# Kernel tuning notes

Measured on AMD Instinct MI355X. Metric: run time of the kernel, lower is better.

## Reference

```python
import jax, jax.numpy as jnp
import numpy as np

NUM_LOC = 20000
T = 24
IN_DIM = 18
H1 = 32
H2 = 32
GRU = 32
PW = 15
E_RAND = 640000


def setup_inputs() -> dict:
    key = jax.random.key(0)
    ks = jax.random.split(key, 32)
    # graph: random edges + self loops so every node has >=1 incoming edge
    edge_src = jnp.concatenate([
        jax.random.randint(ks[0], (E_RAND,), 0, NUM_LOC),
        jnp.arange(NUM_LOC)]).astype(jnp.int32)
    edge_dst = jnp.concatenate([
        jax.random.randint(ks[1], (E_RAND,), 0, NUM_LOC),
        jnp.arange(NUM_LOC)]).astype(jnp.int32)
    dynamic = jax.random.normal(ks[2], (NUM_LOC, T, IN_DIM), dtype=jnp.float32)
    cI = jax.random.uniform(ks[3], (T,), dtype=jnp.float32)
    cR = jax.random.uniform(ks[4], (T,), dtype=jnp.float32)
    I = jax.random.uniform(ks[5], (T,), dtype=jnp.float32)
    R = jax.random.uniform(ks[6], (T,), dtype=jnp.float32)
    N = jax.random.uniform(ks[7], (NUM_LOC, 1), dtype=jnp.float32) * 1e4 + 10.0
    h0 = jax.random.normal(ks[8], (1, GRU), dtype=jnp.float32) * 0.1
    s = 0.1
    # GAT layer 1 (torch Linear convention: weight [out, in], y = x @ W.T + b)
    W1 = jax.random.normal(ks[9], (H1, IN_DIM), dtype=jnp.float32) * s
    b1 = jnp.zeros((H1,), dtype=jnp.float32)
    aW1 = jax.random.normal(ks[10], (1, 2 * H1), dtype=jnp.float32) * s
    ab1 = jnp.zeros((1,), dtype=jnp.float32)
    # GAT layer 2
    W2 = jax.random.normal(ks[11], (H2, H1), dtype=jnp.float32) * s
    b2 = jnp.zeros((H2,), dtype=jnp.float32)
    aW2 = jax.random.normal(ks[12], (1, 2 * H2), dtype=jnp.float32) * s
    ab2 = jnp.zeros((1,), dtype=jnp.float32)
    # GRUCell
    Wih = jax.random.normal(ks[13], (3 * GRU, H2), dtype=jnp.float32) * s
    Whh = jax.random.normal(ks[14], (3 * GRU, GRU), dtype=jnp.float32) * s
    bih = jnp.zeros((3 * GRU,), dtype=jnp.float32)
    bhh = jnp.zeros((3 * GRU,), dtype=jnp.float32)
    # output heads
    WI = jax.random.normal(ks[15], (PW, GRU + 2), dtype=jnp.float32) * s
    bI = jnp.zeros((PW,), dtype=jnp.float32)
    WR = jax.random.normal(ks[16], (PW, GRU + 2), dtype=jnp.float32) * s
    bR = jnp.zeros((PW,), dtype=jnp.float32)
    Ws = jax.random.normal(ks[17], (2, GRU + 2), dtype=jnp.float32) * s
    bs = jnp.zeros((2,), dtype=jnp.float32)
    return {"dynamic": dynamic, "cI": cI, "cR": cR, "N": N, "I": I, "R": R,
            "h0": h0, "W1": W1, "b1": b1, "aW1": aW1, "ab1": ab1,
            "W2": W2, "b2": b2, "aW2": aW2, "ab2": ab2,
            "Wih": Wih, "Whh": Whh, "bih": bih, "bhh": bhh,
            "WI": WI, "bI": bI, "WR": WR, "bR": bR, "Ws": Ws, "bs": bs,
            "edge_src": edge_src, "edge_dst": edge_dst}


def _gat(x, W, b, aW, ab, src, dst):
    # z = fc(x); per-edge attention e = leaky_relu(attn_fc([z_src, z_dst]))
    z = x @ W.T + b                                        # [n, out]
    e = jax.nn.leaky_relu(
        (jnp.concatenate([z[src], z[dst]], axis=1) @ aW.T + ab)[:, 0])  # [E]
    # softmax over incoming edges per destination node
    m = jax.ops.segment_max(e, dst, num_segments=NUM_LOC)
    ex = jnp.exp(e - m[dst])
    den = jax.ops.segment_sum(ex, dst, num_segments=NUM_LOC)
    alpha = ex / den[dst]
    return jax.ops.segment_sum(alpha[:, None] * z[src], dst, num_segments=NUM_LOC)


def reference(dynamic, cI, cR, N, I, R, h0,
              W1, b1, aW1, ab1, W2, b2, aW2, ab2,
              Wih, Whh, bih, bhh, WI, bI, WR, bR, Ws, bs,
              edge_src, edge_dst):
    Nv = N[:, 0]                                          # [num_loc]

    def step(h, inp):
        x_t, cI_t, cR_t, I_t, R_t = inp
        c = jax.nn.elu(_gat(x_t, W1, b1, aW1, ab1, edge_src, edge_dst))
        c = jax.nn.elu(_gat(c, W2, b2, aW2, ab2, edge_src, edge_dst))
        pooled = jnp.max(c, axis=0)[None, :]              # [1, H2]
        # GRUCell
        gi = pooled @ Wih.T + bih
        gh = h @ Whh.T + bhh
        r = jax.nn.sigmoid(gi[:, :GRU] + gh[:, :GRU])
        zg = jax.nn.sigmoid(gi[:, GRU:2 * GRU] + gh[:, GRU:2 * GRU])
        n = jnp.tanh(gi[:, 2 * GRU:] + r * gh[:, 2 * GRU:])
        h_new = (1.0 - zg) * n + zg * h                   # [1, GRU]
        hc = jnp.concatenate([h_new, cI_t.reshape(1, 1), cR_t.reshape(1, 1)], axis=1)
        pred_I = hc @ WI.T + bI                           # [1, PW]
        pred_R = hc @ WR.T + bR
        sir = hc @ Ws.T + bs                              # [1, 2]
        alpha = jax.nn.sigmoid(sir[0, 0])
        beta = jax.nn.sigmoid(sir[0, 1])

        def sir_step(carry, _):
            lI, lR = carry
            lS = Nv - lI - lR
            dI = alpha * lI * (lS / Nv) - beta * lI
            dR = beta * lI
            return (lI + jax.lax.stop_gradient(dI),
                    lR + jax.lax.stop_gradient(dR)), (dI, dR)

        init = (jnp.broadcast_to(I_t, Nv.shape), jnp.broadcast_to(R_t, Nv.shape))
        _, (dIs, dRs) = jax.lax.scan(sir_step, init, None, length=PW)
        # [PW, num_loc] -> [num_loc, PW]
        return h_new, (pred_I, pred_R, dIs.T, dRs.T)

    xs = (jnp.swapaxes(dynamic, 0, 1), cI, cR, I, R)      # time-major
    h_fin, (nI, nR, pI, pR) = jax.lax.scan(step, h0, xs)
    new_I = jnp.transpose(nI, (1, 0, 2))                  # [1, T, PW]
    new_R = jnp.transpose(nR, (1, 0, 2))
    phy_I = jnp.transpose(pI, (1, 0, 2))                  # [num_loc, T, PW]
    phy_R = jnp.transpose(pR, (1, 0, 2))
    return new_I, new_R, phy_I, phy_R, h_fin
```

## Files before the change

### kernel.cpp

```cpp
#include <hip/hip_runtime.h>
#include <hip/hip_fp16.h>
#include <math.h>
#include <float.h>

#define NLOC 20000
#define TT   24
#define NP   12
#define INDIM 18
#define HH   32
#define PWN  15
#define PSTR 32

typedef unsigned short u16;

__device__ __forceinline__ unsigned int fkey(float f) {
    unsigned int b = __float_as_uint(f);
    return b ^ ((unsigned int)((int)b >> 31) | 0x80000000u);
}
__device__ __forceinline__ float funkey(unsigned int u) {
    return (u & 0x80000000u) ? __uint_as_float(u ^ 0x80000000u) : __uint_as_float(~u);
}

__device__ __forceinline__ bool decode_q(int nblk, int swz, int qadd,
                                         int& q, int& blk) {
    if (swz) {
        int F = blockIdx.x;
        int g = F >> 3;
        q = (F & 7) + 8 * (g / nblk);
        blk = g % nblk;
        return q < NP;
    }
    q = qadd + blockIdx.y;
    blk = blockIdx.x;
    return true;
}

__global__ void count_kernel(const int* __restrict__ dst, int* __restrict__ cnt, int E) {
    int e = blockIdx.x * blockDim.x + threadIdx.x;
    if (e < E) atomicAdd(&cnt[dst[e]], 1);
}

__global__ void scan_kernel(const int* __restrict__ cnt, int* __restrict__ row_ptr, int n) {
    __shared__ int sums[1024];
    const int CH = 20;
    int tid = threadIdx.x;
    int base = tid * CH;
    int local[CH];
    int s = 0;
    #pragma unroll
    for (int i = 0; i < CH; ++i) {
        int idx = base + i;
        int v = (idx < n) ? cnt[idx] : 0;
        local[i] = s;
        s += v;
    }
    sums[tid] = s;
    __syncthreads();
    for (int o = 1; o < 1024; o <<= 1) {
        int v = (tid >= o) ? sums[tid - o] : 0;
        __syncthreads();
        sums[tid] += v;
        __syncthreads();
    }
    int pre = (tid > 0) ? sums[tid - 1] : 0;
    #pragma unroll
    for (int i = 0; i < CH; ++i) {
        int idx = base + i;
        if (idx < n) row_ptr[idx] = pre + local[i];
    }
    if (tid == 1023) row_ptr[n] = sums[1023];
}

__global__ void scatter_kernel(const int* __restrict__ src, const int* __restrict__ dst,
                               const int* __restrict__ row_ptr, int* __restrict__ fill,
                               u16* __restrict__ csr_src, int E) {
    int e = blockIdx.x * blockDim.x + threadIdx.x;
    if (e < E) {
        int d = dst[e];
        int pos = row_ptr[d] + atomicAdd(&fill[d], 1);
        csr_src[pos] = (u16)src[e];
    }
}

__global__ void node1_kernel(const float* __restrict__ dyn,
                             const float* __restrict__ W, const float* __restrict__ b,
                             const float* __restrict__ aW, const float* __restrict__ ab,
                             __half2* __restrict__ z2, float2* __restrict__ es2,
                             float2* __restrict__ ed2, int nblk, int swz, int qadd) {
    __shared__ float sW[HH * INDIM];
    __shared__ float sb[HH];
    __shared__ float saW[2 * HH];
    __shared__ float sab;
    int q, blk;
    if (!decode_q(nblk, swz, qadd, q, blk)) return;
    int slice = swz ? q : blockIdx.y;
    int tid = threadIdx.x;
    for (int i = tid; i < HH * INDIM; i += blockDim.x) sW[i] = W[i];
    if (tid < HH) sb[tid] = b[tid];
    if (tid < 2 * HH) saW[tid] = aW[tid];
    if (tid == 0) sab = ab[0];
    __syncthreads();
    int n = blk * blockDim.x + tid;
    if (n >= NLOC) return;
    z2  += (size_t)slice * NLOC * HH;
    es2 += (size_t)slice * NLOC;
    ed2 += (size_t)slice * NLOC;
    const float* xp = dyn + (size_t)n * (TT * INDIM) + (size_t)(2 * q) * INDIM;
    float x0[INDIM], x1[INDIM];
    #pragma unroll
    for (int i = 0; i < INDIM; ++i) { x0[i] = xp[i]; x1[i] = xp[INDIM + i]; }
    float es0 = 0.f, es1 = 0.f, ed0 = sab, ed1 = sab;
    #pragma unroll
    for (int k = 0; k < HH; ++k) {
        float a0 = sb[k], a1 = sb[k];
        #pragma unroll
        for (int i = 0; i < INDIM; ++i) {
            a0 = fmaf(x0[i], sW[k * INDIM + i], a0);
            a1 = fmaf(x1[i], sW[k * INDIM + i], a1);
        }
        z2[(size_t)n * HH + k] = __floats2half2_rn(a0, a1);
        es0 = fmaf(saW[k], a0, es0);       es1 = fmaf(saW[k], a1, es1);
        ed0 = fmaf(saW[HH + k], a0, ed0);  ed1 = fmaf(saW[HH + k], a1, ed1);
    }
    es2[n] = make_float2(es0, es1);
    ed2[n] = make_float2(ed0, ed1);
}

__global__ void node2_kernel(const __half2* __restrict__ c2,
                             const float* __restrict__ W, const float* __restrict__ b,
                             const float* __restrict__ aW, const float* __restrict__ ab,
                             __half2* __restrict__ z2, float2* __restrict__ es2,
                             float2* __restrict__ ed2, int nblk, int swz, int qadd) {
    __shared__ float sW[HH * HH];
    __shared__ float sb[HH];
    __shared__ float saW[2 * HH];
    __shared__ float sab;
    int q, blk;
    if (!decode_q(nblk, swz, qadd, q, blk)) return;
    int slice = swz ? q : blockIdx.y;
    int tid = threadIdx.x;
    for (int i = tid; i < HH * HH; i += blockDim.x) sW[i] = W[i];
    if (tid < HH) sb[tid] = b[tid];
    if (tid < 2 * HH) saW[tid] = aW[tid];
    if (tid == 0) sab = ab[0];
    __syncthreads();
    int n = blk * blockDim.x + tid;
    if (n >= NLOC) return;
    c2  += (size_t)slice * NLOC * HH;
    z2  += (size_t)slice * NLOC * HH;
    es2 += (size_t)slice * NLOC;
    ed2 += (size_t)slice * NLOC;
    float x0[HH], x1[HH];
    const __half2* cp = c2 + (size_t)n * HH;
    #pragma unroll
    for (int i = 0; i < HH; ++i) {
        float2 f = __half22float2(cp[i]);
        x0[i] = f.x; x1[i] = f.y;
    }
    float es0 = 0.f, es1 = 0.f, ed0 = sab, ed1 = sab;
    #pragma unroll
    for (int k = 0; k < HH; ++k) {
        float a0 = sb[k], a1 = sb[k];
        #pragma unroll
        for (int i = 0; i < HH; ++i) {
            a0 = fmaf(x0[i], sW[k * HH + i], a0);
            a1 = fmaf(x1[i], sW[k * HH + i], a1);
        }
        z2[(size_t)n * HH + k] = __floats2half2_rn(a0, a1);
        es0 = fmaf(saW[k], a0, es0);       es1 = fmaf(saW[k], a1, es1);
        ed0 = fmaf(saW[HH + k], a0, ed0);  ed1 = fmaf(saW[HH + k], a1, ed1);
    }
    es2[n] = make_float2(es0, es1);
    ed2[n] = make_float2(ed0, ed1);
}

template<bool WRITE_C, bool POOL>
__global__ void __launch_bounds__(256, 4)
agg_kernel(const int* __restrict__ row_ptr, const u16* __restrict__ csr,
           const __half2* __restrict__ z2t, const float2* __restrict__ es2,
           const float2* __restrict__ ed2, __half2* __restrict__ c2out,
           unsigned int* __restrict__ pooled_u, int nblk, int swz, int qadd) {
    __shared__ int    soff[4][64];
    __shared__ float2 swt[4][64];
    __shared__ float  sred[4][2][HH];
    int q, dblk;
    if (!decode_q(nblk, swz, qadd, q, dblk)) return;
    int slice = swz ? q : blockIdx.y;
    int lane = threadIdx.x & 63;
    int w    = threadIdx.x >> 6;
    int r    = lane >> 3;
    int cg   = lane & 7;
    int d = dblk * 4 + w;
    const __half2* z2q  = z2t + (size_t)slice * NLOC * HH;
    const float2*  es2q = es2 + (size_t)slice * NLOC;
    const float2*  ed2q = ed2 + (size_t)slice * NLOC;

    int beg = 0, end = 0;
    float edd0 = 0.f, edd1 = 0.f;
    if (d < NLOC) {
        beg = row_ptr[d];
        end = row_ptr[d + 1];
        float2 ev = ed2q[d];
        edd0 = ev.x; edd1 = ev.y;
    }
    int deg = end - beg;
    int il = beg + lane;
    bool valid = (il < end);
    int idx_l = valid ? (int)csr[il] : 0;
    float2 esv = es2q[idx_l];
    float e0 = esv.x + edd0; e0 = fmaxf(e0, 0.01f * e0);
    float e1 = esv.y + edd1; e1 = fmaxf(e1, 0.01f * e1);
    float w0 = valid ? __expf(e0) : 0.f;
    float w1 = valid ? __expf(e1) : 0.f;
    soff[w][lane] = idx_l << 7;
    swt[w][lane]  = make_float2(w0, w1);

    const char* zb = (const char*)z2q + cg * 16;
    float2 ac0 = {0.f, 0.f}, ac1 = {0.f, 0.f}, ac2 = {0.f, 0.f}, ac3 = {0.f, 0.f};
    float den0 = 0.f, den1 = 0.f;
    #pragma unroll
    for (int pass = 0; pass < 8; ++pass) {
        int    off = soff[w][pass * 8 + r];
        float2 wv  = swt[w][pass * 8 + r];
        uint4 u = *(const uint4*)(zb + off);
        den0 += wv.x; den1 += wv.y;
        float2 f0 = __half22float2(*(const __half2*)&u.x);
        float2 f1 = __half22float2(*(const __half2*)&u.y);
        float2 f2 = __half22float2(*(const __half2*)&u.z);
        float2 f3 = __half22float2(*(const __half2*)&u.w);
        ac0.x = fmaf(wv.x, f0.x, ac0.x); ac0.y = fmaf(wv.y, f0.y, ac0.y);
        ac1.x = fmaf(wv.x, f1.x, ac1.x); ac1.y = fmaf(wv.y, f1.y, ac1.y);
        ac2.x = fmaf(wv.x, f2.x, ac2.x); ac2.y = fmaf(wv.y, f2.y, ac2.y);
        ac3.x = fmaf(wv.x, f3.x, ac3.x); ac3.y = fmaf(wv.y, f3.y, ac3.y);
    }
    for (int e = 64 + r; e < deg; e += 8) {
        int s2 = (int)csr[beg + e];
        float2 esv2 = es2q[s2];
        float t0 = esv2.x + edd0; t0 = fmaxf(t0, 0.01f * t0);
        float t1 = esv2.y + edd1; t1 = fmaxf(t1, 0.01f * t1);
        float x0 = __expf(t0), x1 = __expf(t1);
        den0 += x0; den1 += x1;
        uint4 u = *(const uint4*)(zb + ((size_t)s2 << 7));
        float2 f0 = __half22float2(*(const __half2*)&u.x);
        float2 f1 = __half22float2(*(const __half2*)&u.y);
        float2 f2 = __half22float2(*(const __half2*)&u.z);
        float2 f3 = __half22float2(*(const __half2*)&u.w);
        ac0.x = fmaf(x0, f0.x, ac0.x); ac0.y = fmaf(x1, f0.y, ac0.y);
        ac1.x = fmaf(x0, f1.x, ac1.x); ac1.y = fmaf(x1, f1.y, ac1.y);
        ac2.x = fmaf(x0, f2.x, ac2.x); ac2.y = fmaf(x1, f2.y, ac2.y);
        ac3.x = fmaf(x0, f3.x, ac3.x); ac3.y = fmaf(x1, f3.y, ac3.y);
    }
    #pragma unroll
    for (int o = 8; o <= 32; o <<= 1) {
        ac0.x += __shfl_xor(ac0.x, o, 64); ac0.y += __shfl_xor(ac0.y, o, 64);
        ac1.x += __shfl_xor(ac1.x, o, 64); ac1.y += __shfl_xor(ac1.y, o, 64);
        ac2.x += __shfl_xor(ac2.x, o, 64); ac2.y += __shfl_xor(ac2.y, o, 64);
        ac3.x += __shfl_xor(ac3.x, o, 64); ac3.y += __shfl_xor(ac3.y, o, 64);
        den0  += __shfl_xor(den0,  o, 64); den1  += __shfl_xor(den1,  o, 64);
    }

    float v00 = -FLT_MAX, v01 = -FLT_MAX, v10 = -FLT_MAX, v11 = -FLT_MAX;
    float v20 = -FLT_MAX, v21 = -FLT_MAX, v30 = -FLT_MAX, v31 = -FLT_MAX;
    if (d < NLOC) {
        float r0 = 1.f / den0, r1 = 1.f / den1;
        v00 = ac0.x * r0; v00 = fmaxf(v00, __expf(fminf(v00, 0.f)) - 1.f);
        v01 = ac0.y * r1; v01 = fmaxf(v01, __expf(fminf(v01, 0.f)) - 1.f);
        v10 = ac1.x * r0; v10 = fmaxf(v10, __expf(fminf(v10, 0.f)) - 1.f);
        v11 = ac1.y * r1; v11 = fmaxf(v11, __expf(fminf(v11, 0.f)) - 1.f);
        v20 = ac2.x * r0; v20 = fmaxf(v20, __expf(fminf(v20, 0.f)) - 1.f);
        v21 = ac2.y * r1; v21 = fmaxf(v21, __expf(fminf(v21, 0.f)) - 1.f);
        v30 = ac3.x * r0; v30 = fmaxf(v30, __expf(fminf(v30, 0.f)) - 1.f);
        v31 = ac3.y * r1; v31 = fmaxf(v31, __expf(fminf(v31, 0.f)) - 1.f);
        if (WRITE_C && r == 0) {
            uint4 pk;
            __half2 h0 = __floats2half2_rn(v00, v01);
            __half2 h1 = __floats2half2_rn(v10, v11);
            __half2 h2 = __floats2half2_rn(v20, v21);
            __half2 h3 = __floats2half2_rn(v30, v31);
            pk.x = *(unsigned int*)&h0; pk.y = *(unsigned int*)&h1;
            pk.z = *(unsigned int*)&h2; pk.w = *(unsigned int*)&h3;
            *(uint4*)((char*)(c2out + (size_t)slice * NLOC * HH + (size_t)d * HH) + cg * 16) = pk;
        }
    }
    if (POOL) {
        if (r == 0) {
            sred[w][0][cg * 4 + 0] = v00; sred[w][1][cg * 4 + 0] = v01;
            sred[w][0][cg * 4 + 1] = v10; sred[w][1][cg * 4 + 1] = v11;
            sred[w][0][cg * 4 + 2] = v20; sred[w][1][cg * 4 + 2] = v21;
            sred[w][0][cg * 4 + 3] = v30; sred[w][1][cg * 4 + 3] = v31;
        }
        __syncthreads();
        if (threadIdx.x < 64) {
            int pp = threadIdx.x >> 5;
            int dim = threadIdx.x & 31;
            float m = fmaxf(fmaxf(sred[0][pp][dim], sred[1][pp][dim]),
                            fmaxf(sred[2][pp][dim], sred[3][pp][dim]));
            atomicMax(&pooled_u[(size_t)((2 * q + pp) * HH + dim) * PSTR], fkey(m));
        }
    }
}

__global__ void gru_all_kernel(const unsigned int* __restrict__ pooled_u,
                               const float* __restrict__ Wih, const float* __restrict__ Whh,
                               const float* __restrict__ bih, const float* __restrict__ bhh,
                               const float* __restrict__ WI, const float* __restrict__ bI,
                               const float* __restrict__ WR, const float* __restrict__ bR,
                               const float* __restrict__ Ws, const float* __restrict__ bs,
                               const float* __restrict__ cIv, const float* __restrict__ cRv,
                               const float* __restrict__ h0, float* __restrict__ abArr,
                               float* __restrict__ out_newI, float* __restrict__ out_newR,
                               float* __restrict__ h_fin) {
    __shared__ float pooled[HH], hs[HH], gi[96], gh[96], hc[34];
    int tid = threadIdx.x;
    float wih_r[HH], whh_r[HH];
    if (tid < 96) {
        #pragma unroll
        for (int k = 0; k < HH; ++k) {
            wih_r[k] = Wih[tid * HH + k];
            whh_r[k] = Whh[tid * HH + k];
        }
    }
    if (tid < HH) hs[tid] = h0[tid];
    __syncthreads();
    for (int t = 0; t < TT; ++t) {
        if (tid < HH) pooled[tid] = funkey(pooled_u[(size_t)(t * HH + tid) * PSTR]);
        __syncthreads();
        if (tid < 96) {
            float a = bih[tid], g = bhh[tid];
            #pragma unroll
            for (int k = 0; k < HH; ++k) {
                a = fmaf(wih_r[k], pooled[k], a);
                g = fmaf(whh_r[k], hs[k], g);
            }
            gi[tid] = a; gh[tid] = g;
        }
        __syncthreads();
        if (tid < HH) {
            float r  = 1.f / (1.f + expf(-(gi[tid] + gh[tid])));
            float zg = 1.f / (1.f + expf(-(gi[HH + tid] + gh[HH + tid])));
            float nn = tanhf(gi[2 * HH + tid] + r * gh[2 * HH + tid]);
            float hn = (1.f - zg) * nn + zg * hs[tid];
            hs[tid] = hn;
            hc[tid] = hn;
        }
        if (tid == 32) hc[32] = cIv[t];
        if (tid == 33) hc[33] = cRv[t];
        __syncthreads();
        if (tid < PWN) {
            float a = bI[tid];
            #pragma unroll
            for (int k = 0; k < 34; ++k) a = fmaf(WI[tid * 34 + k], hc[k], a);
            out_newI[t * PWN + tid] = a;
        } else if (tid >= 32 && tid < 32 + PWN) {
            int p = tid - 32;
            float a = bR[p];
            #pragma unroll
            for (int k = 0; k < 34; ++k) a = fmaf(WR[p * 34 + k], hc[k], a);
            out_newR[t * PWN + p] = a;
        } else if (tid == 64 || tid == 65) {
            int p = tid - 64;
            float a = bs[p];
            #pragma unroll
            for (int k = 0; k < 34; ++k) a = fmaf(Ws[p * 34 + k], hc[k], a);
            abArr[2 * t + p] = 1.f / (1.f + expf(-a));
        }
        __syncthreads();
    }
    if (tid < HH) h_fin[tid] = hs[tid];
}

__global__ void sir_kernel(const float* __restrict__ Nin, const float* __restrict__ Iv,
                           const float* __restrict__ Rv, const float* __restrict__ abArr,
                           float* __restrict__ phyI, float* __restrict__ phyR) {
    int idx = blockIdx.x * blockDim.x + threadIdx.x;
    if (idx >= NLOC * TT) return;
    int n = idx / TT, t = idx - n * TT;
    float Nv = Nin[n];
    float alpha = abArr[2 * t], beta = abArr[2 * t + 1];
    float lI = Iv[t], lR = Rv[t];
    float* oI = phyI + (size_t)idx * PWN;
    float* oR = phyR + (size_t)idx * PWN;
    #pragma unroll
    for (int p = 0; p < PWN; ++p) {
        float lS = Nv - lI - lR;
        float dI = alpha * lI * (lS / Nv) - beta * lI;
        float dR = beta * lI;
        oI[p] = dI;
        oR[p] = dR;
        lI += dI;
        lR += dR;
    }
}

extern "C" void kernel_launch(void* const* d_in, const int* in_sizes, int n_in,
                              void* d_out, int out_size, void* d_ws, size_t ws_size,
                              hipStream_t stream) {
    const float* dynamic = (const float*)d_in[0];
    const float* cIv = (const float*)d_in[1];
    const float* cRv = (const float*)d_in[2];
    const float* Nin = (const float*)d_in[3];
    const float* Iv  = (const float*)d_in[4];
    const float* Rv  = (const float*)d_in[5];
    const float* h0  = (const float*)d_in[6];
    const float* W1  = (const float*)d_in[7];
    const float* b1  = (const float*)d_in[8];
    const float* aW1 = (const float*)d_in[9];
    const float* ab1 = (const float*)d_in[10];
    const float* W2  = (const float*)d_in[11];
    const float* b2  = (const float*)d_in[12];
    const float* aW2 = (const float*)d_in[13];
    const float* ab2 = (const float*)d_in[14];
    const float* Wih = (const float*)d_in[15];
    const float* Whh = (const float*)d_in[16];
    const float* bih = (const float*)d_in[17];
    const float* bhh = (const float*)d_in[18];
    const float* WI  = (const float*)d_in[19];
    const float* bI  = (const float*)d_in[20];
    const float* WR  = (const float*)d_in[21];
    const float* bR  = (const float*)d_in[22];
    const float* Ws  = (const float*)d_in[23];
    const float* bs  = (const float*)d_in[24];
    const int* esrc  = (const int*)d_in[25];
    const int* edst  = (const int*)d_in[26];
    const int E = in_sizes[25];

    float* out = (float*)d_out;
    float* out_newI = out;
    float* out_newR = out + TT * PWN;
    float* phyI = out + 2 * TT * PWN;
    float* phyR = phyI + (size_t)NLOC * TT * PWN;
    float* h_fin = phyR + (size_t)NLOC * TT * PWN;

    char* p = (char*)d_ws;
    int* cnt = (int*)p;                 p += (size_t)NLOC * 4;
    int* fill = (int*)p;                p += (size_t)NLOC * 4;
    int* row_ptr = (int*)p;             p += (size_t)(NLOC + 2) * 4;
    u16* csr = (u16*)p;                 p += ((size_t)E * 2 + 15) & ~(size_t)15;
    unsigned int* pooled_u = (unsigned int*)p; p += (size_t)TT * HH * PSTR * 4;
    float* abArr = (float*)p;           p += (size_t)2 * TT * 4;
    p = (char*)(((size_t)p + 127) & ~(size_t)127);
    size_t fixed_bytes = (size_t)(p - (char*)d_ws);
    size_t per_q_bytes = (size_t)NLOC * HH * 4 * 2 + (size_t)NLOC * 8 * 2;
    int B = 1;
    if (ws_size > fixed_bytes + per_q_bytes)
        B = (int)((ws_size - fixed_bytes) / per_q_bytes);
    if (B > NP) B = NP;
    if (B < 1) B = 1;
    __half2* zb  = (__half2*)p;
    __half2* cb  = zb + (size_t)B * NLOC * HH;
    float2* es2  = (float2*)(cb + (size_t)B * NLOC * HH);
    float2* ed2  = es2 + (size_t)B * NLOC;

    hipMemsetAsync(cnt, 0, (size_t)2 * NLOC * 4, stream);
    hipMemsetAsync(pooled_u, 0, (size_t)TT * HH * PSTR * 4, stream);

    int egrid = (E + 255) / 256;
    count_kernel<<<egrid, 256, 0, stream>>>(edst, cnt, E);
    scan_kernel<<<1, 1024, 0, stream>>>(cnt, row_ptr, NLOC);
    scatter_kernel<<<egrid, 256, 0, stream>>>(esrc, edst, row_ptr, fill, csr, E);

    const int NBLK_N = (NLOC + 255) / 256;
    const int NBLK_A = (NLOC + 3) / 4;

    if (B >= NP) {
        dim3 ng(NBLK_N * 16), ag(NBLK_A * 16);
        node1_kernel<<<ng, 256, 0, stream>>>(dynamic, W1, b1, aW1, ab1,
                                             zb, es2, ed2, NBLK_N, 1, 0);
        agg_kernel<true, false><<<ag, 256, 0, stream>>>(
            row_ptr, csr, zb, es2, ed2, cb, pooled_u, NBLK_A, 1, 0);
        node2_kernel<<<ng, 256, 0, stream>>>(cb, W2, b2, aW2, ab2,
                                             zb, es2, ed2, NBLK_N, 1, 0);
        agg_kernel<false, true><<<ag, 256, 0, stream>>>(
            row_ptr, csr, zb, es2, ed2, nullptr, pooled_u, NBLK_A, 1, 0);
    } else {
        for (int qbase = 0; qbase < NP; qbase += B) {
            int Bc = NP - qbase; if (Bc > B) Bc = B;
            dim3 ng(NBLK_N, Bc), ag(NBLK_A, Bc);
            node1_kernel<<<ng, 256, 0, stream>>>(dynamic, W1, b1, aW1, ab1,
                                                 zb, es2, ed2, NBLK_N, 0, qbase);
            agg_kernel<true, false><<<ag, 256, 0, stream>>>(
                row_ptr, csr, zb, es2, ed2, cb, pooled_u, NBLK_A, 0, qbase);
            node2_kernel<<<ng, 256, 0, stream>>>(cb, W2, b2, aW2, ab2,
                                                 zb, es2, ed2, NBLK_N, 0, qbase);
            agg_kernel<false, true><<<ag, 256, 0, stream>>>(
                row_ptr, csr, zb, es2, ed2, nullptr, pooled_u, NBLK_A, 0, qbase);
        }
    }

    gru_all_kernel<<<1, 128, 0, stream>>>(pooled_u, Wih, Whh, bih, bhh,
                                          WI, bI, WR, bR, Ws, bs, cIv, cRv,
                                          h0, abArr, out_newI, out_newR, h_fin);
    sir_kernel<<<(NLOC * TT + 255) / 256, 256, 0, stream>>>(Nin, Iv, Rv, abArr, phyI, phyR);
}
```

Measured before the change: 637.8 us.

## Batch four timesteps per slice in GAT node and aggregation kernels

Packs four timesteps per node row (256-byte rows of half2 pairs) instead of two, so each gathered neighbour row and CSR index serves four timesteps. This halves the number of slices and the repeated CSR/row_ptr traversal and edge-softmax index loads across the aggregation passes. The block swizzle is changed to a contiguous chunked mapping across the 8 XCD-interleaved block slots. Each aggregation lane now handles 16 column groups with fewer rows per pass, and per-thread work in the node kernels doubles, which may raise register pressure.

Result: slower. 1.064 ms (+66.8%).

```diff
diff --git a/kernel.cpp b/kernel.cpp
--- a/kernel.cpp
+++ b/kernel.cpp
@@ -5,7 +5,7 @@
 
 #define NLOC 20000
 #define TT   24
-#define NP   12
+#define NQ   6
 #define INDIM 18
 #define HH   32
 #define PWN  15
@@ -21,14 +21,15 @@
     return (u & 0x80000000u) ? __uint_as_float(u ^ 0x80000000u) : __uint_as_float(~u);
 }
 
-__device__ __forceinline__ bool decode_q(int nblk, int swz, int qadd,
-                                         int& q, int& blk) {
+__device__ __forceinline__ bool decode_q6(int nblk, int swz, int qadd,
+                                          int& q, int& blk) {
     if (swz) {
-        int F = blockIdx.x;
-        int g = F >> 3;
-        q = (F & 7) + 8 * (g / nblk);
-        blk = g % nblk;
-        return q < NP;
+        int CH = (NQ * nblk + 7) >> 3;
+        int x = blockIdx.x & 7, g = blockIdx.x >> 3;
+        int B = x * CH + g;
+        if (B >= NQ * nblk) return false;
+        q = B / nblk; blk = B - q * nblk;
+        return true;
     }
     q = qadd + blockIdx.y;
     blk = blockIdx.x;
@@ -85,14 +86,14 @@
 __global__ void node1_kernel(const float* __restrict__ dyn,
                              const float* __restrict__ W, const float* __restrict__ b,
                              const float* __restrict__ aW, const float* __restrict__ ab,
-                             __half2* __restrict__ z2, float2* __restrict__ es2,
-                             float2* __restrict__ ed2, int nblk, int swz, int qadd) {
+                             char* __restrict__ z4, float4* __restrict__ es4,
+                             float4* __restrict__ ed4, int nblk, int swz, int qadd) {
+    int q, blk;
+    if (!decode_q6(nblk, swz, qadd, q, blk)) return;
     __shared__ float sW[HH * INDIM];
     __shared__ float sb[HH];
     __shared__ float saW[2 * HH];
     __shared__ float sab;
-    int q, blk;
-    if (!decode_q(nblk, swz, qadd, q, blk)) return;
     int slice = swz ? q : blockIdx.y;
     int tid = threadIdx.x;
     for (int i = tid; i < HH * INDIM; i += blockDim.x) sW[i] = W[i];
@@ -102,41 +103,47 @@
     __syncthreads();
     int n = blk * blockDim.x + tid;
     if (n >= NLOC) return;
-    z2  += (size_t)slice * NLOC * HH;
-    es2 += (size_t)slice * NLOC;
-    ed2 += (size_t)slice * NLOC;
-    const float* xp = dyn + (size_t)n * (TT * INDIM) + (size_t)(2 * q) * INDIM;
-    float x0[INDIM], x1[INDIM];
-    #pragma unroll
-    for (int i = 0; i < INDIM; ++i) { x0[i] = xp[i]; x1[i] = xp[INDIM + i]; }
-    float es0 = 0.f, es1 = 0.f, ed0 = sab, ed1 = sab;
-    #pragma unroll
-    for (int k = 0; k < HH; ++k) {
-        float a0 = sb[k], a1 = sb[k];
+    char* zrow = z4 + ((size_t)slice * NLOC + n) * 256;
+    const float* xp = dyn + (size_t)n * (TT * INDIM) + (size_t)(4 * q) * INDIM;
+    float esv[4], edv[4];
+    #pragma unroll
+    for (int tt = 0; tt < 2; ++tt) {
+        const float* x0 = xp + (2 * tt) * INDIM;
+        const float* x1 = x0 + INDIM;
+        float xr0[INDIM], xr1[INDIM];
         #pragma unroll
-        for (int i = 0; i < INDIM; ++i) {
-            a0 = fmaf(x0[i], sW[k * INDIM + i], a0);
-            a1 = fmaf(x1[i], sW[k * INDIM + i], a1);
-        }
-        z2[(size_t)n * HH + k] = __floats2half2_rn(a0, a1);
-        es0 = fmaf(saW[k], a0, es0);       es1 = fmaf(saW[k], a1, es1);
-        ed0 = fmaf(saW[HH + k], a0, ed0);  ed1 = fmaf(saW[HH + k], a1, ed1);
-    }
-    es2[n] = make_float2(es0, es1);
-    ed2[n] = make_float2(ed0, ed1);
-}
-
-__global__ void node2_kernel(const __half2* __restrict__ c2,
+        for (int i = 0; i < INDIM; ++i) { xr0[i] = x0[i]; xr1[i] = x1[i]; }
+        float es0 = 0.f, es1 = 0.f, ed0 = sab, ed1 = sab;
+        #pragma unroll
+        for (int k = 0; k < HH; ++k) {
+            float a0 = sb[k], a1 = sb[k];
+            #pragma unroll
+            for (int i = 0; i < INDIM; ++i) {
+                a0 = fmaf(xr0[i], sW[k * INDIM + i], a0);
+                a1 = fmaf(xr1[i], sW[k * INDIM + i], a1);
+            }
+            *(__half2*)(zrow + k * 8 + tt * 4) = __floats2half2_rn(a0, a1);
+            es0 = fmaf(saW[k], a0, es0);       es1 = fmaf(saW[k], a1, es1);
+            ed0 = fmaf(saW[HH + k], a0, ed0);  ed1 = fmaf(saW[HH + k], a1, ed1);
+        }
+        esv[2 * tt] = es0; esv[2 * tt + 1] = es1;
+        edv[2 * tt] = ed0; edv[2 * tt + 1] = ed1;
+    }
+    es4[(size_t)slice * NLOC + n] = make_float4(esv[0], esv[1], esv[2], esv[3]);
+    ed4[(size_t)slice * NLOC + n] = make_float4(edv[0], edv[1], edv[2], edv[3]);
+}
+
+__global__ void node2_kernel(const char* __restrict__ c4,
                              const float* __restrict__ W, const float* __restrict__ b,
                              const float* __restrict__ aW, const float* __restrict__ ab,
-                             __half2* __restrict__ z2, float2* __restrict__ es2,
-                             float2* __restrict__ ed2, int nblk, int swz, int qadd) {
+                             char* __restrict__ z4, float4* __restrict__ es4,
+                             float4* __restrict__ ed4, int nblk, int swz, int qadd) {
+    int q, blk;
+    if (!decode_q6(nblk, swz, qadd, q, blk)) return;
     __shared__ float sW[HH * HH];
     __shared__ float sb[HH];
     __shared__ float saW[2 * HH];
     __shared__ float sab;
-    int q, blk;
-    if (!decode_q(nblk, swz, qadd, q, blk)) return;
     int slice = swz ? q : blockIdx.y;
     int tid = threadIdx.x;
     for (int i = tid; i < HH * HH; i += blockDim.x) sW[i] = W[i];
@@ -146,156 +153,166 @@
     __syncthreads();
     int n = blk * blockDim.x + tid;
     if (n >= NLOC) return;
-    c2  += (size_t)slice * NLOC * HH;
-    z2  += (size_t)slice * NLOC * HH;
-    es2 += (size_t)slice * NLOC;
-    ed2 += (size_t)slice * NLOC;
-    float x0[HH], x1[HH];
-    const __half2* cp = c2 + (size_t)n * HH;
-    #pragma unroll
-    for (int i = 0; i < HH; ++i) {
-        float2 f = __half22float2(cp[i]);
-        x0[i] = f.x; x1[i] = f.y;
-    }
-    float es0 = 0.f, es1 = 0.f, ed0 = sab, ed1 = sab;
-    #pragma unroll
-    for (int k = 0; k < HH; ++k) {
-        float a0 = sb[k], a1 = sb[k];
+    const char* crow = c4 + ((size_t)slice * NLOC + n) * 256;
+    char* zrow = z4 + ((size_t)slice * NLOC + n) * 256;
+    float esv[4], edv[4];
+    #pragma unroll
+    for (int tt = 0; tt < 2; ++tt) {
+        float x0[HH], x1[HH];
         #pragma unroll
         for (int i = 0; i < HH; ++i) {
-            a0 = fmaf(x0[i], sW[k * HH + i], a0);
-            a1 = fmaf(x1[i], sW[k * HH + i], a1);
-        }
-        z2[(size_t)n * HH + k] = __floats2half2_rn(a0, a1);
-        es0 = fmaf(saW[k], a0, es0);       es1 = fmaf(saW[k], a1, es1);
-        ed0 = fmaf(saW[HH + k], a0, ed0);  ed1 = fmaf(saW[HH + k], a1, ed1);
-    }
-    es2[n] = make_float2(es0, es1);
-    ed2[n] = make_float2(ed0, ed1);
+            float2 f = __half22float2(*(const __half2*)(crow + i * 8 + tt * 4));
+            x0[i] = f.x; x1[i] = f.y;
+        }
+        float es0 = 0.f, es1 = 0.f, ed0 = sab, ed1 = sab;
+        #pragma unroll
+        for (int k = 0; k < HH; ++k) {
+            float a0 = sb[k], a1 = sb[k];
+            #pragma unroll
+            for (int i = 0; i < HH; ++i) {
+                a0 = fmaf(x0[i], sW[k * HH + i], a0);
+                a1 = fmaf(x1[i], sW[k * HH + i], a1);
+            }
+            *(__half2*)(zrow + k * 8 + tt * 4) = __floats2half2_rn(a0, a1);
+            es0 = fmaf(saW[k], a0, es0);       es1 = fmaf(saW[k], a1, es1);
+            ed0 = fmaf(saW[HH + k], a0, ed0);  ed1 = fmaf(saW[HH + k], a1, ed1);
+        }
+        esv[2 * tt] = es0; esv[2 * tt + 1] = es1;
+        edv[2 * tt] = ed0; edv[2 * tt + 1] = ed1;
+    }
+    es4[(size_t)slice * NLOC + n] = make_float4(esv[0], esv[1], esv[2], esv[3]);
+    ed4[(size_t)slice * NLOC + n] = make_float4(edv[0], edv[1], edv[2], edv[3]);
 }
 
 template<bool WRITE_C, bool POOL>
 __global__ void __launch_bounds__(256, 4)
 agg_kernel(const int* __restrict__ row_ptr, const u16* __restrict__ csr,
-           const __half2* __restrict__ z2t, const float2* __restrict__ es2,
-           const float2* __restrict__ ed2, __half2* __restrict__ c2out,
+           const char* __restrict__ z4t, const float4* __restrict__ es4,
+           const float4* __restrict__ ed4, char* __restrict__ c4out,
            unsigned int* __restrict__ pooled_u, int nblk, int swz, int qadd) {
+    int q, dblk;
+    if (!decode_q6(nblk, swz, qadd, q, dblk)) return;
     __shared__ int    soff[4][64];
-    __shared__ float2 swt[4][64];
-    __shared__ float  sred[4][2][HH];
-    int q, dblk;
-    if (!decode_q(nblk, swz, qadd, q, dblk)) return;
+    __shared__ float4 swt[4][64];
+    __shared__ float  sred[4][4][HH];
     int slice = swz ? q : blockIdx.y;
     int lane = threadIdx.x & 63;
     int w    = threadIdx.x >> 6;
-    int r    = lane >> 3;
-    int cg   = lane & 7;
+    int r    = lane >> 4;
+    int cg   = lane & 15;
     int d = dblk * 4 + w;
-    const __half2* z2q  = z2t + (size_t)slice * NLOC * HH;
-    const float2*  es2q = es2 + (size_t)slice * NLOC;
-    const float2*  ed2q = ed2 + (size_t)slice * NLOC;
+    const char*   z4q  = z4t + (size_t)slice * NLOC * 256;
+    const float4* es4q = es4 + (size_t)slice * NLOC;
+    const float4* ed4q = ed4 + (size_t)slice * NLOC;
 
     int beg = 0, end = 0;
-    float edd0 = 0.f, edd1 = 0.f;
+    float4 edd = {0.f, 0.f, 0.f, 0.f};
     if (d < NLOC) {
         beg = row_ptr[d];
         end = row_ptr[d + 1];
-        float2 ev = ed2q[d];
-        edd0 = ev.x; edd1 = ev.y;
+        edd = ed4q[d];
     }
     int deg = end - beg;
     int il = beg + lane;
     bool valid = (il < end);
     int idx_l = valid ? (int)csr[il] : 0;
-    float2 esv = es2q[idx_l];
-    float e0 = esv.x + edd0; e0 = fmaxf(e0, 0.01f * e0);
-    float e1 = esv.y + edd1; e1 = fmaxf(e1, 0.01f * e1);
+    float4 esv = es4q[idx_l];
+    float e0 = esv.x + edd.x; e0 = fmaxf(e0, 0.01f * e0);
+    float e1 = esv.y + edd.y; e1 = fmaxf(e1, 0.01f * e1);
+    float e2 = esv.z + edd.z; e2 = fmaxf(e2, 0.01f * e2);
+    float e3 = esv.w + edd.w; e3 = fmaxf(e3, 0.01f * e3);
     float w0 = valid ? __expf(e0) : 0.f;
     float w1 = valid ? __expf(e1) : 0.f;
-    soff[w][lane] = idx_l << 7;
-    swt[w][lane]  = make_float2(w0, w1);
-
-    const char* zb = (const char*)z2q + cg * 16;
-    float2 ac0 = {0.f, 0.f}, ac1 = {0.f, 0.f}, ac2 = {0.f, 0.f}, ac3 = {0.f, 0.f};
-    float den0 = 0.f, den1 = 0.f;
-    #pragma unroll
-    for (int pass = 0; pass < 8; ++pass) {
-        int    off = soff[w][pass * 8 + r];
-        float2 wv  = swt[w][pass * 8 + r];
+    float w2 = valid ? __expf(e2) : 0.f;
+    float w3 = valid ? __expf(e3) : 0.f;
+    soff[w][lane] = idx_l << 8;
+    swt[w][lane]  = make_float4(w0, w1, w2, w3);
+
+    const char* zb = z4q + cg * 16;
+    float2 a0t01 = {0.f,0.f}, a0t23 = {0.f,0.f}, a1t01 = {0.f,0.f}, a1t23 = {0.f,0.f};
+    float2 den01 = {0.f,0.f}, den23 = {0.f,0.f};
+    #pragma unroll
+    for (int pass = 0; pass < 16; ++pass) {
+        int    off = soff[w][pass * 4 + r];
+        float4 wv  = swt[w][pass * 4 + r];
         uint4 u = *(const uint4*)(zb + off);
-        den0 += wv.x; den1 += wv.y;
-        float2 f0 = __half22float2(*(const __half2*)&u.x);
-        float2 f1 = __half22float2(*(const __half2*)&u.y);
-        float2 f2 = __half22float2(*(const __half2*)&u.z);
-        float2 f3 = __half22float2(*(const __half2*)&u.w);
-        ac0.x = fmaf(wv.x, f0.x, ac0.x); ac0.y = fmaf(wv.y, f0.y, ac0.y);
-        ac1.x = fmaf(wv.x, f1.x, ac1.x); ac1.y = fmaf(wv.y, f1.y, ac1.y);
-        ac2.x = fmaf(wv.x, f2.x, ac2.x); ac2.y = fmaf(wv.y, f2.y, ac2.y);
-        ac3.x = fmaf(wv.x, f3.x, ac3.x); ac3.y = fmaf(wv.y, f3.y, ac3.y);
-    }
-    for (int e = 64 + r; e < deg; e += 8) {
+        den01.x += wv.x; den01.y += wv.y; den23.x += wv.z; den23.y += wv.w;
+        float2 f0a = __half22float2(*(const __half2*)&u.x);
+        float2 f0b = __half22float2(*(const __half2*)&u.y);
+        float2 f1a = __half22float2(*(const __half2*)&u.z);
+        float2 f1b = __half22float2(*(const __half2*)&u.w);
+        a0t01.x = fmaf(wv.x, f0a.x, a0t01.x); a0t01.y = fmaf(wv.y, f0a.y, a0t01.y);
+        a0t23.x = fmaf(wv.z, f0b.x, a0t23.x); a0t23.y = fmaf(wv.w, f0b.y, a0t23.y);
+        a1t01.x = fmaf(wv.x, f1a.x, a1t01.x); a1t01.y = fmaf(wv.y, f1a.y, a1t01.y);
+        a1t23.x = fmaf(wv.z, f1b.x, a1t23.x); a1t23.y = fmaf(wv.w, f1b.y, a1t23.y);
+    }
+    for (int e = 64 + r; e < deg; e += 4) {
         int s2 = (int)csr[beg + e];
-        float2 esv2 = es2q[s2];
-        float t0 = esv2.x + edd0; t0 = fmaxf(t0, 0.01f * t0);
-        float t1 = esv2.y + edd1; t1 = fmaxf(t1, 0.01f * t1);
-        float x0 = __expf(t0), x1 = __expf(t1);
-        den0 += x0; den1 += x1;
-        uint4 u = *(const uint4*)(zb + ((size_t)s2 << 7));
-        float2 f0 = __half22float2(*(const __half2*)&u.x);
-        float2 f1 = __half22float2(*(const __half2*)&u.y);
-        float2 f2 = __half22float2(*(const __half2*)&u.z);
-        float2 f3 = __half22float2(*(const __half2*)&u.w);
-        ac0.x = fmaf(x0, f0.x, ac0.x); ac0.y = fmaf(x1, f0.y, ac0.y);
-        ac1.x = fmaf(x0, f1.x, ac1.x); ac1.y = fmaf(x1, f1.y, ac1.y);
-        ac2.x = fmaf(x0, f2.x, ac2.x); ac2.y = fmaf(x1, f2.y, ac2.y);
-        ac3.x = fmaf(x0, f3.x, ac3.x); ac3.y = fmaf(x1, f3.y, ac3.y);
-    }
-    #pragma unroll
-    for (int o = 8; o <= 32; o <<= 1) {
-        ac0.x += __shfl_xor(ac0.x, o, 64); ac0.y += __shfl_xor(ac0.y, o, 64);
-        ac1.x += __shfl_xor(ac1.x, o, 64); ac1.y += __shfl_xor(ac1.y, o, 64);
-        ac2.x += __shfl_xor(ac2.x, o, 64); ac2.y += __shfl_xor(ac2.y, o, 64);
-        ac3.x += __shfl_xor(ac3.x, o, 64); ac3.y += __shfl_xor(ac3.y, o, 64);
-        den0  += __shfl_xor(den0,  o, 64); den1  += __shfl_xor(den1,  o, 64);
-    }
-
-    float v00 = -FLT_MAX, v01 = -FLT_MAX, v10 = -FLT_MAX, v11 = -FLT_MAX;
-    float v20 = -FLT_MAX, v21 = -FLT_MAX, v30 = -FLT_MAX, v31 = -FLT_MAX;
+        float4 ev = es4q[s2];
+        float t0 = ev.x + edd.x; t0 = fmaxf(t0, 0.01f * t0);
+        float t1 = ev.y + edd.y; t1 = fmaxf(t1, 0.01f * t1);
+        float t2 = ev.z + edd.z; t2 = fmaxf(t2, 0.01f * t2);
+        float t3 = ev.w + edd.w; t3 = fmaxf(t3, 0.01f * t3);
+        float x0 = __expf(t0), x1 = __expf(t1), x2 = __expf(t2), x3 = __expf(t3);
+        den01.x += x0; den01.y += x1; den23.x += x2; den23.y += x3;
+        uint4 u = *(const uint4*)(zb + ((size_t)s2 << 8));
+        float2 f0a = __half22float2(*(const __half2*)&u.x);
+        float2 f0b = __half22float2(*(const __half2*)&u.y);
+        float2 f1a = __half22float2(*(const __half2*)&u.z);
+        float2 f1b = __half22float2(*(const __half2*)&u.w);
+        a0t01.x = fmaf(x0, f0a.x, a0t01.x); a0t01.y = fmaf(x1, f0a.y, a0t01.y);
+        a0t23.x = fmaf(x2, f0b.x, a0t23.x); a0t23.y = fmaf(x3, f0b.y, a0t23.y);
+        a1t01.x = fmaf(x0, f1a.x, a1t01.x); a1t01.y = fmaf(x1, f1a.y, a1t01.y);
+        a1t23.x = fmaf(x2, f1b.x, a1t23.x); a1t23.y = fmaf(x3, f1b.y, a1t23.y);
+    }
+    #pragma unroll
+    for (int o = 16; o <= 32; o <<= 1) {
+        a0t01.x += __shfl_xor(a0t01.x, o, 64); a0t01.y += __shfl_xor(a0t01.y, o, 64);
+        a0t23.x += __shfl_xor(a0t23.x, o, 64); a0t23.y += __shfl_xor(a0t23.y, o, 64);
+        a1t01.x += __shfl_xor(a1t01.x, o, 64); a1t01.y += __shfl_xor(a1t01.y, o, 64);
+        a1t23.x += __shfl_xor(a1t23.x, o, 64); a1t23.y += __shfl_xor(a1t23.y, o, 64);
+        den01.x += __shfl_xor(den01.x, o, 64); den01.y += __shfl_xor(den01.y, o, 64);
+        den23.x += __shfl_xor(den23.x, o, 64); den23.y += __shfl_xor(den23.y, o, 64);
+    }
+
+    float v00 = -FLT_MAX, v01 = -FLT_MAX, v02 = -FLT_MAX, v03 = -FLT_MAX;
+    float v10 = -FLT_MAX, v11 = -FLT_MAX, v12 = -FLT_MAX, v13 = -FLT_MAX;
     if (d < NLOC) {
-        float r0 = 1.f / den0, r1 = 1.f / den1;
-        v00 = ac0.x * r0; v00 = fmaxf(v00, __expf(fminf(v00, 0.f)) - 1.f);
-        v01 = ac0.y * r1; v01 = fmaxf(v01, __expf(fminf(v01, 0.f)) - 1.f);
-        v10 = ac1.x * r0; v10 = fmaxf(v10, __expf(fminf(v10, 0.f)) - 1.f);
-        v11 = ac1.y * r1; v11 = fmaxf(v11, __expf(fminf(v11, 0.f)) - 1.f);
-        v20 = ac2.x * r0; v20 = fmaxf(v20, __expf(fminf(v20, 0.f)) - 1.f);
-        v21 = ac2.y * r1; v21 = fmaxf(v21, __expf(fminf(v21, 0.f)) - 1.f);
-        v30 = ac3.x * r0; v30 = fmaxf(v30, __expf(fminf(v30, 0.f)) - 1.f);
-        v31 = ac3.y * r1; v31 = fmaxf(v31, __expf(fminf(v31, 0.f)) - 1.f);
+        float r0 = 1.f / den01.x, r1 = 1.f / den01.y;
+        float r2 = 1.f / den23.x, r3 = 1.f / den23.y;
+        v00 = a0t01.x * r0; v00 = fmaxf(v00, __expf(fminf(v00, 0.f)) - 1.f);
+        v01 = a0t01.y * r1; v01 = fmaxf(v01, __expf(fminf(v01, 0.f)) - 1.f);
+        v02 = a0t23.x * r2; v02 = fmaxf(v02, __expf(fminf(v02, 0.f)) - 1.f);
+        v03 = a0t23.y * r3; v03 = fmaxf(v03, __expf(fminf(v03, 0.f)) - 1.f);
+        v10 = a1t01.x * r0; v10 = fmaxf(v10, __expf(fminf(v10, 0.f)) - 1.f);
+        v11 = a1t01.y * r1; v11 = fmaxf(v11, __expf(fminf(v11, 0.f)) - 1.f);
+        v12 = a1t23.x * r2; v12 = fmaxf(v12, __expf(fminf(v12, 0.f)) - 1.f);
+        v13 = a1t23.y * r3; v13 = fmaxf(v13, __expf(fminf(v13, 0.f)) - 1.f);
         if (WRITE_C && r == 0) {
             uint4 pk;
             __half2 h0 = __floats2half2_rn(v00, v01);
-            __half2 h1 = __floats2half2_rn(v10, v11);
-            __half2 h2 = __floats2half2_rn(v20, v21);
-            __half2 h3 = __floats2half2_rn(v30, v31);
+            __half2 h1 = __floats2half2_rn(v02, v03);
+            __half2 h2 = __floats2half2_rn(v10, v11);
+            __half2 h3 = __floats2half2_rn(v12, v13);
             pk.x = *(unsigned int*)&h0; pk.y = *(unsigned int*)&h1;
             pk.z = *(unsigned int*)&h2; pk.w = *(unsigned int*)&h3;
-            *(uint4*)((char*)(c2out + (size_t)slice * NLOC * HH + (size_t)d * HH) + cg * 16) = pk;
+            *(uint4*)(c4out + ((size_t)slice * NLOC + d) * 256 + cg * 16) = pk;
         }
     }
     if (POOL) {
         if (r == 0) {
-            sred[w][0][cg * 4 + 0] = v00; sred[w][1][cg * 4 + 0] = v01;
-            sred[w][0][cg * 4 + 1] = v10; sred[w][1][cg * 4 + 1] = v11;
-            sred[w][0][cg * 4 + 2] = v20; sred[w][1][cg * 4 + 2] = v21;
-            sred[w][0][cg * 4 + 3] = v30; sred[w][1][cg * 4 + 3] = v31;
-        }
-        __syncthreads();
-        if (threadIdx.x < 64) {
+            sred[w][0][cg * 2 + 0] = v00; sred[w][1][cg * 2 + 0] = v01;
+            sred[w][2][cg * 2 + 0] = v02; sred[w][3][cg * 2 + 0] = v03;
+            sred[w][0][cg * 2 + 1] = v10; sred[w][1][cg * 2 + 1] = v11;
+            sred[w][2][cg * 2 + 1] = v12; sred[w][3][cg * 2 + 1] = v13;
+        }
+        __syncthreads();
+        if (threadIdx.x < 128) {
             int pp = threadIdx.x >> 5;
             int dim = threadIdx.x & 31;
             float m = fmaxf(fmaxf(sred[0][pp][dim], sred[1][pp][dim]),
                             fmaxf(sred[2][pp][dim], sred[3][pp][dim]));
-            atomicMax(&pooled_u[(size_t)((2 * q + pp) * HH + dim) * PSTR], fkey(m));
+            atomicMax(&pooled_u[(size_t)((4 * q + pp) * HH + dim) * PSTR], fkey(m));
         }
     }
 }
@@ -438,18 +455,18 @@
     u16* csr = (u16*)p;                 p += ((size_t)E * 2 + 15) & ~(size_t)15;
     unsigned int* pooled_u = (unsigned int*)p; p += (size_t)TT * HH * PSTR * 4;
     float* abArr = (float*)p;           p += (size_t)2 * TT * 4;
-    p = (char*)(((size_t)p + 127) & ~(size_t)127);
+    p = (char*)(((size_t)p + 255) & ~(size_t)255);
     size_t fixed_bytes = (size_t)(p - (char*)d_ws);
-    size_t per_q_bytes = (size_t)NLOC * HH * 4 * 2 + (size_t)NLOC * 8 * 2;
+    size_t per_q_bytes = (size_t)NLOC * (256 + 256 + 16 + 16);
     int B = 1;
     if (ws_size > fixed_bytes + per_q_bytes)
         B = (int)((ws_size - fixed_bytes) / per_q_bytes);
-    if (B > NP) B = NP;
+    if (B > NQ) B = NQ;
     if (B < 1) B = 1;
-    __half2* zb  = (__half2*)p;
-    __half2* cb  = zb + (size_t)B * NLOC * HH;
-    float2* es2  = (float2*)(cb + (size_t)B * NLOC * HH);
-    float2* ed2  = es2 + (size_t)B * NLOC;
+    char* zb   = p;
+    char* cb   = zb + (size_t)B * NLOC * 256;
+    float4* es4 = (float4*)(cb + (size_t)B * NLOC * 256);
+    float4* ed4 = es4 + (size_t)B * NLOC;
 
     hipMemsetAsync(cnt, 0, (size_t)2 * NLOC * 4, stream);
     hipMemsetAsync(pooled_u, 0, (size_t)TT * HH * PSTR * 4, stream);
@@ -461,29 +478,31 @@
 
     const int NBLK_N = (NLOC + 255) / 256;
     const int NBLK_A = (NLOC + 3) / 4;
-
-    if (B >= NP) {
-        dim3 ng(NBLK_N * 16), ag(NBLK_A * 16);
+    const int GRID_N = 8 * ((NQ * NBLK_N + 7) / 8);
+    const int GRID_A = 8 * ((NQ * NBLK_A + 7) / 8);
+
+    if (B >= NQ) {
+        dim3 ng(GRID_N), ag(GRID_A);
         node1_kernel<<<ng, 256, 0, stream>>>(dynamic, W1, b1, aW1, ab1,
-                                             zb, es2, ed2, NBLK_N, 1, 0);
+                                             zb, es4, ed4, NBLK_N, 1, 0);
         agg_kernel<true, false><<<ag, 256, 0, stream>>>(
-            row_ptr, csr, zb, es2, ed2, cb, pooled_u, NBLK_A, 1, 0);
+            row_ptr, csr, zb, es4, ed4, cb, pooled_u, NBLK_A, 1, 0);
         node2_kernel<<<ng, 256, 0, stream>>>(cb, W2, b2, aW2, ab2,
-                                             zb, es2, ed2, NBLK_N, 1, 0);
+                                             zb, es4, ed4, NBLK_N, 1, 0);
         agg_kernel<false, true><<<ag, 256, 0, stream>>>(
-            row_ptr, csr, zb, es2, ed2, nullptr, pooled_u, NBLK_A, 1, 0);
+            row_ptr, csr, zb, es4, ed4, nullptr, pooled_u, NBLK_A, 1, 0);
     } else {
-        for (int qbase = 0; qbase < NP; qbase += B) {
-            int Bc = NP - qbase; if (Bc > B) Bc = B;
+        for (int qbase = 0; qbase < NQ; qbase += B) {
+            int Bc = NQ - qbase; if (Bc > B) Bc = B;
             dim3 ng(NBLK_N, Bc), ag(NBLK_A, Bc);
             node1_kernel<<<ng, 256, 0, stream>>>(dynamic, W1, b1, aW1, ab1,
-                                                 zb, es2, ed2, NBLK_N, 0, qbase);
+                                                 zb, es4, ed4, NBLK_N, 0, qbase);
             agg_kernel<true, false><<<ag, 256, 0, stream>>>(
-                row_ptr, csr, zb, es2, ed2, cb, pooled_u, NBLK_A, 0, qbase);
+                row_ptr, csr, zb, es4, ed4, cb, pooled_u, NBLK_A, 0, qbase);
             node2_kernel<<<ng, 256, 0, stream>>>(cb, W2, b2, aW2, ab2,
-                                                 zb, es2, ed2, NBLK_N, 0, qbase);
+                                                 zb, es4, ed4, NBLK_N, 0, qbase);
             agg_kernel<false, true><<<ag, 256, 0, stream>>>(
-                row_ptr, csr, zb, es2, ed2, nullptr, pooled_u, NBLK_A, 0, qbase);
+                row_ptr, csr, zb, es4, ed4, nullptr, pooled_u, NBLK_A, 0, qbase);
         }
     }
 
```
